# Kernel tuning notes

Measured on AMD Instinct MI355X. Metric: run time of the kernel, lower is better.

The kernel has to match this reference:

```python
import jax, jax.numpy as jnp
import numpy as np

HEADS, DIM_HEAD, LANDMARKS, PINV_ITERS = 8, 64, 256, 6
SCALE = DIM_HEAD ** -0.5
D, L, B, N_IN = 512, 768, 4, 6170


def dwconv(x, w, b, ph, pw):
    # x: [B,C,H,W]; w: [C,1,kh,kw] depthwise (groups=C)
    C = x.shape[1]
    y = jax.lax.conv_general_dilated(x, w, (1, 1), ((ph, ph), (pw, pw)),
                                     feature_group_count=C,
                                     dimension_numbers=('NCHW', 'OIHW', 'NCHW'))
    if b is not None:
        y = y + b[None, :, None, None]
    return y


def layer_norm(x, g, b, eps=1e-5):
    mu = x.mean(-1, keepdims=True)
    var = jnp.mean((x - mu) ** 2, -1, keepdims=True)
    return (x - mu) * jax.lax.rsqrt(var + eps) * g + b


def pinv_iter(a, iters):
    # Moore-Penrose iterative pseudo-inverse (lucidrains), global max normalization
    col = jnp.abs(a).sum(-1).max()
    row = jnp.abs(a).sum(-2).max()
    z = jnp.swapaxes(a, -1, -2) / (col * row)
    I = jnp.eye(a.shape[-1], dtype=a.dtype)
    for _ in range(iters):
        az = a @ z
        z = 0.25 * z @ (13 * I - az @ (15 * I - az @ (7 * I - az)))
    return z


def nystrom_attention(x, qkv_w, out_w, out_b, res_w):
    b, n, _ = x.shape
    m = LANDMARKS
    pad = (m - n % m) % m
    xp = jnp.pad(x, ((0, 0), (pad, 0), (0, 0)))  # pad at front, like F.pad
    N = n + pad
    q, k, v = jnp.split(xp @ qkv_w, 3, axis=-1)
    to_heads = lambda t: t.reshape(b, N, HEADS, DIM_HEAD).transpose(0, 2, 1, 3)
    q, k, v = to_heads(q) * SCALE, to_heads(k), to_heads(v)
    l = N // m
    q_l = q.reshape(b, HEADS, m, l, DIM_HEAD).mean(3)  # landmark means
    k_l = k.reshape(b, HEADS, m, l, DIM_HEAD).mean(3)
    sim1 = jnp.einsum('bhnd,bhmd->bhnm', q, k_l)
    sim2 = jnp.einsum('bhid,bhjd->bhij', q_l, k_l)
    sim3 = jnp.einsum('bhmd,bhnd->bhmn', q_l, k)
    a1 = jax.nn.softmax(sim1, -1)
    a2 = jax.nn.softmax(sim2, -1)
    a3 = jax.nn.softmax(sim3, -1)
    out = (a1 @ pinv_iter(a2, PINV_ITERS)) @ (a3 @ v)
    out = out + dwconv(v, res_w, None, 16, 0)  # depthwise (33,1) conv over seq per head
    out = out.transpose(0, 2, 1, 3).reshape(b, N, HEADS * DIM_HEAD)
    out = out @ out_w + out_b
    return out[:, -n:]


def ppeg(x, w7, b7, w5, b5, w3, b3, H, W):
    Bx, _, C = x.shape
    cls = x[:, :1]
    feat = x[:, 1:].transpose(0, 2, 1).reshape(Bx, C, H, W)
    y = feat + dwconv(feat, w7, b7, 3, 3) + dwconv(feat, w5, b5, 2, 2) + dwconv(feat, w3, b3, 1, 1)
    y = y.reshape(Bx, C, H * W).transpose(0, 2, 1)
    return jnp.concatenate([cls, y], axis=1)


def setup_inputs() -> dict:
    key = jax.random.key(0)
    ks = jax.random.split(key, 24)
    nrm = lambda k, shape, s=0.02: jax.random.normal(k, shape, jnp.float32) * s
    zeros = lambda *s: jnp.zeros(s, jnp.float32)
    ones = lambda *s: jnp.ones(s, jnp.float32)
    return {
        'x': jax.random.normal(ks[0], (B, N_IN, L), jnp.float32),
        'fc1_w': nrm(ks[1], (L, D)), 'fc1_b': zeros(D),
        'cls_token': nrm(ks[2], (1, 1, D)),
        'l1_norm_g': ones(D), 'l1_norm_b': zeros(D),
        'l1_qkv_w': nrm(ks[3], (D, 3 * D)), 'l1_out_w': nrm(ks[4], (D, D)), 'l1_out_b': zeros(D),
        'l1_res_w': nrm(ks[5], (HEADS, 1, 33, 1)),
        'ct_w7': nrm(ks[6], (D, 1, 7, 7)), 'ct_b7': zeros(D),
        'ct_w5': nrm(ks[7], (D, 1, 5, 5)), 'ct_b5': zeros(D),
        'ct_w3': nrm(ks[8], (D, 1, 3, 3)), 'ct_b3': zeros(D),
        'pth_w7': nrm(ks[9], (D, 1, 7, 7)), 'pth_b7': zeros(D),
        'pth_w5': nrm(ks[10], (D, 1, 5, 5)), 'pth_b5': zeros(D),
        'pth_w3': nrm(ks[11], (D, 1, 3, 3)), 'pth_b3': zeros(D),
        'l2_norm_g': ones(D), 'l2_norm_b': zeros(D),
        'l2_qkv_w': nrm(ks[12], (D, 3 * D)), 'l2_out_w': nrm(ks[13], (D, D)), 'l2_out_b': zeros(D),
        'l2_res_w': nrm(ks[14], (HEADS, 1, 33, 1)),
        'norm_g': ones(D), 'norm_b': zeros(D),
    }


def reference(x, fc1_w, fc1_b, cls_token,
              l1_norm_g, l1_norm_b, l1_qkv_w, l1_out_w, l1_out_b, l1_res_w,
              ct_w7, ct_b7, ct_w5, ct_b5, ct_w3, ct_b3,
              pth_w7, pth_b7, pth_w5, pth_b5, pth_w3, pth_b3,
              l2_norm_g, l2_norm_b, l2_qkv_w, l2_out_w, l2_out_b, l2_res_w,
              norm_g, norm_b):
    h = jax.nn.relu(x.astype(jnp.float32) @ fc1_w + fc1_b)  # [B,N,D]
    h_ct = h[:, 10:10 + 160, :]
    h_pth = h[:, 10 + 160:, :]
    # square-pad each modality (static shapes -> Python ints)
    Hc = h_ct.shape[1]
    sc = int(np.ceil(np.sqrt(Hc)))
    h_ct = jnp.concatenate([h_ct, h_ct[:, :sc * sc - Hc, :]], 1)
    n_ct = h_ct.shape[1]
    Hp = h_pth.shape[1]
    sp = int(np.ceil(np.sqrt(Hp)))
    h_pth = jnp.concatenate([h_pth, h_pth[:, :sp * sp - Hp, :]], 1)
    h = jnp.concatenate([h[:, :10, :], h_ct, h_pth], 1)
    Bx = h.shape[0]
    cls = jnp.broadcast_to(cls_token, (Bx, 1, cls_token.shape[-1]))
    h = jnp.concatenate([cls, h], 1)
    # layer 1
    h = h + nystrom_attention(layer_norm(h, l1_norm_g, l1_norm_b), l1_qkv_w, l1_out_w, l1_out_b, l1_res_w)
    # PPEG per modality
    hc = jnp.concatenate([h[:, :1, :], h[:, 1 + 10:1 + 10 + n_ct, :]], 1)
    hp = jnp.concatenate([h[:, :1, :], h[:, 1 + 10 + n_ct:, :]], 1)
    hc = ppeg(hc, ct_w7, ct_b7, ct_w5, ct_b5, ct_w3, ct_b3, sc, sc)
    hp = ppeg(hp, pth_w7, pth_b7, pth_w5, pth_b5, pth_w3, pth_b3, sp, sp)
    h = jnp.concatenate([h[:, :1 + 10, :], hc[:, 1:, :], hp[:, 1:, :]], 1)
    # layer 2
    h = h + nystrom_attention(layer_norm(h, l2_norm_g, l2_norm_b), l2_qkv_w, l2_out_w, l2_out_b, l2_res_w)
    return layer_norm(h, norm_g, norm_b)[:, 0]
```

## Files before the change

### kernel.cpp

```cpp
#include <hip/hip_runtime.h>
#include <hip/hip_bf16.h>
#include <cstdint>

#define B_   4
#define NTOK 6264
#define NPAD 6400
#define D_   512
#define NH   8
#define NLM  256
#define N0   6170
#define PADF (NPAD - NTOK)
#define MFC1 24704
#define QE   ((long long)NPAD * 1536)

typedef __attribute__((ext_vector_type(8))) short short8_t;
typedef __attribute__((ext_vector_type(4))) float float4_t;

__device__ __forceinline__ ushort f2b(float x){
  __hip_bfloat16 h = __float2bfloat16(x); return *(ushort*)&h;
}
__device__ __forceinline__ float b2f(ushort u){
  __hip_bfloat16 h = *(__hip_bfloat16*)&u; return __bfloat162float(h);
}
__device__ __forceinline__ float gload(const void* p, int bf, long long i){
  return bf ? __bfloat162float(((const __hip_bfloat16*)p)[i]) : ((const float*)p)[i];
}
__device__ __forceinline__ void atomicMaxF(float* a, float v){
  atomicMax((int*)a, __float_as_int(v));
}
__device__ __forceinline__ void gl_lds16(const void* g, void* l){
  __builtin_amdgcn_global_load_lds(
      (const __attribute__((address_space(1))) void*)g,
      (__attribute__((address_space(3))) void*)l, 16, 0, 0);
}

struct GB {
  const __hip_bfloat16* A; const __hip_bfloat16* Bm; void* C; const float* bias;
  int M, N, K, lda, ldb, ldc;
  long long aSO, aSI; int aIn;
  long long bSO, bSI; int bIn;
  long long cSO, cSI; int cIn;
  float beta; int cbf, relu, ksp, klen;
};

template<int BN>
__global__ __launch_bounds__(256) void gemm_bt(GB p){
  __shared__ __align__(16) __hip_bfloat16 As[128*64];
  __shared__ __align__(16) __hip_bfloat16 Bs[BN*64];
  int zz = blockIdx.z;
  int z = zz / p.ksp, ks = zz - z*p.ksp;
  int k0 = ks * p.klen;
  int kend = k0 + p.klen; if (kend > p.K) kend = p.K;
  const __hip_bfloat16* A  = p.A  + (long long)(z/p.aIn)*p.aSO + (long long)(z%p.aIn)*p.aSI;
  const __hip_bfloat16* Bm = p.Bm + (long long)(z/p.bIn)*p.bSO + (long long)(z%p.bIn)*p.bSI;
  long long cOff = (long long)(z/p.cIn)*p.cSO + (long long)(z%p.cIn)*p.cSI;
  int rowBase = blockIdx.y*128, colBase = blockIdx.x*BN;
  int t = threadIdx.x, lane = t & 63;
  int wv = __builtin_amdgcn_readfirstlane(t >> 6);
  int lm = lane & 15, lq = lane >> 4;
  int dr = lane >> 3, dc = lane & 7;
  constexpr int NF = (BN == 128) ? 4 : 2;
  int wm = (wv >> 1) * 64;
  int wn = (BN == 128) ? (wv & 1) * 64 : (wv & 1) * 32;
  float4_t acc[4][NF];
  #pragma unroll
  for (int mi = 0; mi < 4; mi++)
    #pragma unroll
    for (int nf = 0; nf < NF; nf++) acc[mi][nf] = (float4_t)0.f;

  for (int kb = k0; kb < kend; kb += 64){
    #pragma unroll
    for (int d = 0; d < 4; d++){
      int rg = wv*4 + d;
      int row = rg*8 + dr;
      int cc = dc ^ (row & 7);
      gl_lds16(A + (long long)(rowBase + row)*p.lda + kb + cc*8, &As[rg*8*64]);
    }
    #pragma unroll
    for (int d = 0; d < BN/32; d++){
      int rg = wv*(BN/32) + d;
      int row = rg*8 + dr;
      int cc = dc ^ (row & 7);
      gl_lds16(Bm + (long long)(colBase + row)*p.ldb + kb + cc*8, &Bs[rg*8*64]);
    }
    __syncthreads();
    short8_t af[2][4]; short8_t bfv[2][NF];
    #pragma unroll
    for (int ks2 = 0; ks2 < 2; ks2++){
      #pragma unroll
      for (int mi = 0; mi < 4; mi++){
        int r = wm + mi*16 + lm;
        int s = (ks2*4 + lq) ^ (r & 7);
        af[ks2][mi] = *(const short8_t*)&As[r*64 + s*8];
      }
      #pragma unroll
      for (int nf = 0; nf < NF; nf++){
        int r = wn + nf*16 + lm;
        int s = (ks2*4 + lq) ^ (r & 7);
        bfv[ks2][nf] = *(const short8_t*)&Bs[r*64 + s*8];
      }
    }
    #pragma unroll
    for (int ks2 = 0; ks2 < 2; ks2++)
      #pragma unroll
      for (int mi = 0; mi < 4; mi++)
        #pragma unroll
        for (int nf = 0; nf < NF; nf++)
          acc[mi][nf] = __builtin_amdgcn_mfma_f32_16x16x32_bf16(af[ks2][mi], bfv[ks2][nf], acc[mi][nf], 0, 0, 0);
    __syncthreads();
  }
  #pragma unroll
  for (int mi = 0; mi < 4; mi++){
    #pragma unroll
    for (int nf = 0; nf < NF; nf++){
      int c = colBase + wn + nf*16 + lm;
      #pragma unroll
      for (int r = 0; r < 4; r++){
        int m = rowBase + wm + mi*16 + lq*4 + r;
        if (m >= p.M) continue;
        float v = p.beta * acc[mi][nf][r];
        long long ci = cOff + (long long)m*p.ldc + c;
        if (p.ksp > 1){
          atomicAdd((float*)p.C + ci, v);
        } else {
          if (p.bias) v += p.bias[c];
          if (p.relu) v = fmaxf(v, 0.f);
          if (p.cbf) ((__hip_bfloat16*)p.C)[ci] = __float2bfloat16(v);
          else       ((float*)p.C)[ci] = v;
        }
      }
    }
  }
}

struct GS {
  const __hip_bfloat16* A; const __hip_bfloat16* B;
  __hip_bfloat16* outN; __hip_bfloat16* outT;
  long long PS;
  float scale, alphaT, sT;
};

__global__ __launch_bounds__(256) void gemm_bts(GS p){
  __shared__ __align__(16) __hip_bfloat16 Ah[64*64];
  __shared__ __align__(16) __hip_bfloat16 Al[64*64];
  __shared__ __align__(16) __hip_bfloat16 Bh[64*64];
  __shared__ __align__(16) __hip_bfloat16 Bl[64*64];
  int z = blockIdx.z;
  long long zo = (long long)z * 65536;
  const __hip_bfloat16* A = p.A + zo;
  const __hip_bfloat16* B = p.B + zo;
  int rowBase = blockIdx.y*64, colBase = blockIdx.x*64;
  int t = threadIdx.x, lane = t & 63;
  int wv = __builtin_amdgcn_readfirstlane(t >> 6);
  int lm = lane & 15, lq = lane >> 4;
  int dr = lane >> 3, dc = lane & 7;
  int wm = (wv >> 1) * 32, wn = (wv & 1) * 32;
  float4_t acc[2][2];
  #pragma unroll
  for (int mi = 0; mi < 2; mi++){ acc[mi][0] = (float4_t)0.f; acc[mi][1] = (float4_t)0.f; }

  for (int kb = 0; kb < 256; kb += 64){
    #pragma unroll
    for (int d = 0; d < 2; d++){
      int rg = wv*2 + d;
      int row = rg*8 + dr;
      int cc = dc ^ (row & 7);
      gl_lds16(A +        (long long)(rowBase + row)*256 + kb + cc*8, &Ah[rg*8*64]);
      gl_lds16(A + p.PS + (long long)(rowBase + row)*256 + kb + cc*8, &Al[rg*8*64]);
      gl_lds16(B +        (long long)(colBase + row)*256 + kb + cc*8, &Bh[rg*8*64]);
      gl_lds16(B + p.PS + (long long)(colBase + row)*256 + kb + cc*8, &Bl[rg*8*64]);
    }
    __syncthreads();
    #pragma unroll
    for (int ks2 = 0; ks2 < 2; ks2++){
      short8_t ah[2], al2[2], bh[2], bl2[2];
      #pragma unroll
      for (int mi = 0; mi < 2; mi++){
        int r = wm + mi*16 + lm;
        int s = (ks2*4 + lq) ^ (r & 7);
        ah[mi]  = *(const short8_t*)&Ah[r*64 + s*8];
        al2[mi] = *(const short8_t*)&Al[r*64 + s*8];
      }
      #pragma unroll
      for (int nf = 0; nf < 2; nf++){
        int r = wn + nf*16 + lm;
        int s = (ks2*4 + lq) ^ (r & 7);
        bh[nf]  = *(const short8_t*)&Bh[r*64 + s*8];
        bl2[nf] = *(const short8_t*)&Bl[r*64 + s*8];
      }
      #pragma unroll
      for (int mi = 0; mi < 2; mi++)
        #pragma unroll
        for (int nf = 0; nf < 2; nf++){
          acc[mi][nf] = __builtin_amdgcn_mfma_f32_16x16x32_bf16(ah[mi],  bh[nf],  acc[mi][nf], 0, 0, 0);
          acc[mi][nf] = __builtin_amdgcn_mfma_f32_16x16x32_bf16(ah[mi],  bl2[nf], acc[mi][nf], 0, 0, 0);
          acc[mi][nf] = __builtin_amdgcn_mfma_f32_16x16x32_bf16(al2[mi], bh[nf],  acc[mi][nf], 0, 0, 0);
        }
    }
    __syncthreads();
  }
  #pragma unroll
  for (int mi = 0; mi < 2; mi++){
    #pragma unroll
    for (int nf = 0; nf < 2; nf++){
      int c = colBase + wn + nf*16 + lm;
      #pragma unroll
      for (int r = 0; r < 4; r++){
        int m = rowBase + wm + mi*16 + lq*4 + r;
        float v = p.scale * acc[mi][nf][r];
        if (p.outN){
          __hip_bfloat16 hi = __float2bfloat16(v);
          p.outN[zo + (long long)m*256 + c] = hi;
          p.outN[p.PS + zo + (long long)m*256 + c] = __float2bfloat16(v - __bfloat162float(hi));
        }
        if (p.outT){
          float w = p.alphaT * (m == c ? 1.f : 0.f) + p.sT * v;
          __hip_bfloat16 hi = __float2bfloat16(w);
          p.outT[zo + (long long)c*256 + m] = hi;
          p.outT[p.PS + zo + (long long)c*256 + m] = __float2bfloat16(w - __bfloat162float(hi));
        }
      }
    }
  }
}

__global__ __launch_bounds__(256) void sim1_fused(const __hip_bfloat16* QKV,
    const __hip_bfloat16* KL, const __hip_bfloat16* ZVT, float* OUT1){
  __shared__ __align__(16) __hip_bfloat16 Ps[64*256];
  int z = blockIdx.y, b = z >> 3, h = z & 7;
  int n0 = blockIdx.x * 64;
  int t = threadIdx.x, lane = t & 63;
  int wv = __builtin_amdgcn_readfirstlane(t >> 6);
  int lm = lane & 15, lq = lane >> 4;
  const __hip_bfloat16* Qb = QKV + (long long)b*QE + h*64;
  const __hip_bfloat16* Kb = KL + (long long)z*NLM*64;
  const __hip_bfloat16* Zb = ZVT + (long long)z*64*256;

  float4_t sacc[16];
  #pragma unroll
  for (int nf = 0; nf < 16; nf++) sacc[nf] = (float4_t)0.f;
  int qrow = n0 + wv*16 + lm;
  #pragma unroll
  for (int ks = 0; ks < 2; ks++){
    short8_t a = *(const short8_t*)(Qb + (long long)qrow*1536 + ks*32 + lq*8);
    #pragma unroll
    for (int nf = 0; nf < 16; nf++){
      short8_t bb = *(const short8_t*)(Kb + (nf*16 + lm)*64 + ks*32 + lq*8);
      sacc[nf] = __builtin_amdgcn_mfma_f32_16x16x32_bf16(a, bb, sacc[nf], 0, 0, 0);
    }
  }
  #pragma unroll
  for (int reg = 0; reg < 4; reg++){
    float mx = -1e30f;
    #pragma unroll
    for (int nf = 0; nf < 16; nf++){
      sacc[nf][reg] *= 0.125f;
      mx = fmaxf(mx, sacc[nf][reg]);
    }
    #pragma unroll
    for (int m = 1; m <= 8; m <<= 1) mx = fmaxf(mx, __shfl_xor(mx, m));
    float sum = 0.f;
    #pragma unroll
    for (int nf = 0; nf < 16; nf++){
      float e = __expf(sacc[nf][reg] - mx);
      sacc[nf][reg] = e; sum += e;
    }
    #pragma unroll
    for (int m = 1; m <= 8; m <<= 1) sum += __shfl_xor(sum, m);
    float inv = 1.f / sum;
    int row = wv*16 + lq*4 + reg;
    #pragma unroll
    for (int nf = 0; nf < 16; nf++){
      int col = nf*16 + lm;
      int chunk = (col >> 3) ^ (row & 7);
      Ps[row*256 + chunk*8 + (col & 7)] = __float2bfloat16(sacc[nf][reg] * inv);
    }
  }
  float4_t oacc[4];
  #pragma unroll
  for (int nf = 0; nf < 4; nf++) oacc[nf] = (float4_t)0.f;
  int prow = wv*16 + lm;
  #pragma unroll
  for (int ks = 0; ks < 8; ks++){
    int chunk = (ks*4 + lq) ^ (lm & 7);
    short8_t a = *(const short8_t*)&Ps[prow*256 + chunk*8];
    #pragma unroll
    for (int nf = 0; nf < 4; nf++){
      short8_t bb = *(const short8_t*)(Zb + (nf*16 + lm)*256 + ks*32 + lq*8);
      oacc[nf] = __builtin_amdgcn_mfma_f32_16x16x32_bf16(a, bb, oacc[nf], 0, 0, 0);
    }
  }
  #pragma unroll
  for (int nf = 0; nf < 4; nf++){
    #pragma unroll
    for (int reg = 0; reg < 4; reg++){
      int tok = n0 + wv*16 + lq*4 + reg;
      OUT1[((long long)b*NPAD + tok)*D_ + h*64 + nf*16 + lm] = oacc[nf][reg];
    }
  }
}

template<int LEN>
__global__ __launch_bounds__(256) void softmax_rows_b(__hip_bfloat16* S){
  constexpr int VPT = LEN / 256;
  __hip_bfloat16* p = S + (long long)blockIdx.x * LEN;
  int t = threadIdx.x;
  float v[VPT]; float m = -1e30f;
  #pragma unroll
  for (int q = 0; q < VPT; q++){ v[q] = __bfloat162float(p[t + 256*q]); m = fmaxf(m, v[q]); }
  __shared__ float red[256];
  red[t] = m; __syncthreads();
  for (int s = 128; s; s >>= 1){ if (t < s) red[t] = fmaxf(red[t], red[t+s]); __syncthreads(); }
  m = red[0]; __syncthreads();
  float sum = 0.f;
  #pragma unroll
  for (int q = 0; q < VPT; q++){ v[q] = __expf(v[q] - m); sum += v[q]; }
  red[t] = sum; __syncthreads();
  for (int s = 128; s; s >>= 1){ if (t < s) red[t] += red[t+s]; __syncthreads(); }
  float inv = 1.f / red[0];
  #pragma unroll
  for (int q = 0; q < VPT; q++) p[t + 256*q] = __float2bfloat16(v[q] * inv);
}

__global__ __launch_bounds__(256) void softmax256_split(float* S, __hip_bfloat16* P, long long PS){
  long long row = blockIdx.x;
  float* p = S + row * 256;
  int t = threadIdx.x;
  float v = p[t];
  __shared__ float red[256];
  red[t] = v; __syncthreads();
  for (int s = 128; s; s >>= 1){ if (t < s) red[t] = fmaxf(red[t], red[t+s]); __syncthreads(); }
  float m = red[0]; __syncthreads();
  float e = __expf(v - m);
  red[t] = e; __syncthreads();
  for (int s = 128; s; s >>= 1){ if (t < s) red[t] += red[t+s]; __syncthreads(); }
  float r = e / red[0];
  p[t] = r;
  __hip_bfloat16 hi = __float2bfloat16(r);
  P[row*256 + t] = hi;
  P[PS + row*256 + t] = __float2bfloat16(r - __bfloat162float(hi));
}

__global__ __launch_bounds__(256) void ln_pad(const float* H, __hip_bfloat16* X,
                                              const float* g, const float* bb){
  int p = blockIdx.x, b = blockIdx.y, t = threadIdx.x;
  __hip_bfloat16* xo = X + ((long long)b * NPAD + p) * D_;
  if (p < PADF){ xo[t] = __float2bfloat16(0.f); xo[t + 256] = __float2bfloat16(0.f); return; }
  const float* hi = H + ((long long)b * NTOK + (p - PADF)) * D_;
  float x0 = hi[t], x1 = hi[t + 256];
  __shared__ float r1[256], r2[256];
  r1[t] = x0 + x1; r2[t] = x0*x0 + x1*x1;
  __syncthreads();
  for (int s = 128; s; s >>= 1){ if (t < s){ r1[t] += r1[t+s]; r2[t] += r2[t+s]; } __syncthreads(); }
  float mu = r1[0] * (1.f / D_);
  float var = r2[0] * (1.f / D_) - mu*mu;
  float rs = rsqrtf(var + 1e-5f);
  xo[t]       = __float2bfloat16((x0 - mu) * rs * g[t]       + bb[t]);
  xo[t + 256] = __float2bfloat16((x1 - mu) * rs * g[t + 256] + bb[t + 256]);
}

__global__ __launch_bounds__(256) void final_ln(const float* H, const float* g,
                                                const float* bb, float* out){
  int b = blockIdx.x, t = threadIdx.x;
  const float* hi = H + (long long)b * NTOK * D_;
  float x0 = hi[t], x1 = hi[t + 256];
  __shared__ float r1[256], r2[256];
  r1[t] = x0 + x1; r2[t] = x0*x0 + x1*x1;
  __syncthreads();
  for (int s = 128; s; s >>= 1){ if (t < s){ r1[t] += r1[t+s]; r2[t] += r2[t+s]; } __syncthreads(); }
  float mu = r1[0] * (1.f / D_);
  float var = r2[0] * (1.f / D_) - mu*mu;
  float rs = rsqrtf(var + 1e-5f);
  out[b*D_ + t]       = (x0 - mu) * rs * g[t]       + bb[t];
  out[b*D_ + t + 256] = (x1 - mu) * rs * g[t + 256] + bb[t + 256];
}

__global__ __launch_bounds__(256) void build_h(const float* h0, const float* cls, float* H){
  int tpos = blockIdx.x, b = blockIdx.y, t = threadIdx.x;
  float* dst = H + ((long long)b * NTOK + tpos) * D_;
  if (tpos == 0){ dst[t] = cls[t]; dst[t + 256] = cls[t + 256]; return; }
  int i = tpos - 1, src;
  if (i < 10)        src = i;
  else if (i < 179){ int j = i - 10;  src = 10  + (j < 160  ? j : j - 160);  }
  else             { int j = i - 179; src = 170 + (j < 6000 ? j : j - 6000); }
  const float* s = h0 + ((long long)b * N0 + src) * D_;
  dst[t] = s[t]; dst[t + 256] = s[t + 256];
}

__global__ __launch_bounds__(256) void cvt_pad_x(const float* x, __hip_bfloat16* Xb){
  int row = blockIdx.x, t = threadIdx.x;
  __hip_bfloat16* o = Xb + (long long)row * 768;
  if (row >= B_*N0){ o[t] = __float2bfloat16(0.f); o[t+256] = __float2bfloat16(0.f); o[t+512] = __float2bfloat16(0.f); return; }
  const float* s = x + (long long)row * 768;
  o[t]     = __float2bfloat16(s[t]);
  o[t+256] = __float2bfloat16(s[t+256]);
  o[t+512] = __float2bfloat16(s[t+512]);
}

__global__ __launch_bounds__(256) void tr_cvt(const void* in, int inbf, int ldin,
    long long iSO, long long iSI, int iIn, __hip_bfloat16* outp, long long oSO,
    int R, int C){
  __shared__ float sm[32][33];
  int z = blockIdx.z;
  long long ib = (long long)(z/iIn)*iSO + (long long)(z%iIn)*iSI;
  int r0 = blockIdx.y*32, c0 = blockIdx.x*32;
  int tx = threadIdx.x & 31, ty = threadIdx.x >> 5;
  for (int rr = ty; rr < 32; rr += 8)
    sm[rr][tx] = gload(in, inbf, ib + (long long)(r0+rr)*ldin + c0 + tx);
  __syncthreads();
  for (int cc = ty; cc < 32; cc += 8)
    outp[z*oSO + (long long)(c0+cc)*R + r0 + tx] = __float2bfloat16(sm[tx][cc]);
}

__global__ __launch_bounds__(256) void landmarks2(const __hip_bfloat16* QKV,
                                                  __hip_bfloat16* QL, __hip_bfloat16* KL){
  int j = blockIdx.x, b = blockIdx.y, t = threadIdx.x;
  const __hip_bfloat16* base = QKV + ((long long)b * NPAD + j*25) * 1536;
  float q0 = 0.f, q1 = 0.f, k0 = 0.f, k1 = 0.f;
  #pragma unroll 5
  for (int i = 0; i < 25; i++){
    const __hip_bfloat16* row = base + (long long)i*1536;
    q0 += __bfloat162float(row[t]);
    q1 += __bfloat162float(row[t + 256]);
    k0 += __bfloat162float(row[512 + t]);
    k1 += __bfloat162float(row[512 + t + 256]);
  }
  int h0 = t >> 6, d0 = t & 63;
  int h1 = (t + 256) >> 6, d1 = (t + 256) & 63;
  QL[((long long)(b*8 + h0) * NLM + j) * 64 + d0] = __float2bfloat16(q0 * 0.005f);
  QL[((long long)(b*8 + h1) * NLM + j) * 64 + d1] = __float2bfloat16(q1 * 0.005f);
  KL[((long long)(b*8 + h0) * NLM + j) * 64 + d0] = __float2bfloat16(k0 * 0.04f);
  KL[((long long)(b*8 + h1) * NLM + j) * 64 + d1] = __float2bfloat16(k1 * 0.04f);
}

__global__ void init_sc(float* sc){ sc[0] = 0.f; sc[1] = 0.f; }
__global__ __launch_bounds__(256) void fillz(float* p, int n){
  int i = blockIdx.x*256 + threadIdx.x; if (i < n) p[i] = 0.f;
}

__global__ __launch_bounds__(256) void colsum_max(const float* A2, float* sc){
  int z = blockIdx.x, t = threadIdx.x;
  const float* a = A2 + (long long)z * 65536;
  float s = 0.f;
  for (int i = 0; i < 256; i++) s += fabsf(a[i*256 + t]);
  __shared__ float red[256];
  red[t] = s; __syncthreads();
  for (int st = 128; st; st >>= 1){ if (t < st) red[t] = fmaxf(red[t], red[t+st]); __syncthreads(); }
  if (t == 0) atomicMaxF(sc + 0, red[0]);
}

__global__ __launch_bounds__(256) void rowsum_max(const float* A2, float* sc){
  int z = blockIdx.x, t = threadIdx.x, w = t >> 6, l = t & 63;
  const float* a = A2 + (long long)z * 65536;
  float mx = 0.f;
  for (int i = w*64; i < (w+1)*64; i++){
    float s = fabsf(a[i*256 + l]) + fabsf(a[i*256 + l + 64])
            + fabsf(a[i*256 + l + 128]) + fabsf(a[i*256 + l + 192]);
    for (int m = 32; m; m >>= 1) s += __shfl_xor(s, m);
    mx = fmaxf(mx, s);
  }
  __shared__ float red[4];
  if (l == 0) red[w] = mx;
  __syncthreads();
  if (t == 0) atomicMaxF(sc + 1, fmaxf(fmaxf(red[0], red[1]), fmaxf(red[2], red[3])));
}

__global__ __launch_bounds__(256) void zinit_split(const float* A2,
    __hip_bfloat16* ZN, __hip_bfloat16* ZT, long long PS, const float* sc){
  int j = blockIdx.x, z = blockIdx.y, i = threadIdx.x;
  float inv = 1.f / (sc[0] * sc[1]);
  float v = A2[(long long)z*65536 + i*256 + j] * inv;
  __hip_bfloat16 hi = __float2bfloat16(v);
  __hip_bfloat16 lo = __float2bfloat16(v - __bfloat162float(hi));
  long long zo = (long long)z*65536;
  ZN[zo + j*256 + i] = hi; ZN[PS + zo + j*256 + i] = lo;
  ZT[zo + i*256 + j] = hi; ZT[PS + zo + i*256 + j] = lo;
}

__global__ __launch_bounds__(256) void dwconv_cvt2(const __hip_bfloat16* QKV, const float* rw,
                                                   const float* OUT1, __hip_bfloat16* OUT1b){
  int t = threadIdx.x;
  int n = blockIdx.x*4 + (t >> 6);
  int b = blockIdx.y;
  int ch0 = (t & 63) * 8;
  int h = (t & 63) >> 3;
  float w[33];
  #pragma unroll
  for (int k = 0; k < 33; k++) w[k] = rw[h*33 + k];
  float acc[8] = {};
  const __hip_bfloat16* Vb = QKV + (long long)b * NPAD * 1536 + 1024 + ch0;
  #pragma unroll
  for (int k = 0; k < 33; k++){
    int nn = n + k - 16;
    if (nn < 0 || nn >= NPAD) continue;
    short8_t v8 = *(const short8_t*)(Vb + (long long)nn * 1536);
    #pragma unroll
    for (int j = 0; j < 8; j++) acc[j] += w[k] * b2f((ushort)v8[j]);
  }
  long long idx = ((long long)b * NPAD + n) * D_ + ch0;
  float4 o0 = *(const float4*)(OUT1 + idx);
  float4 o1 = *(const float4*)(OUT1 + idx + 4);
  short8_t o;
  o[0] = (short)f2b(o0.x + acc[0]); o[1] = (short)f2b(o0.y + acc[1]);
  o[2] = (short)f2b(o0.z + acc[2]); o[3] = (short)f2b(o0.w + acc[3]);
  o[4] = (short)f2b(o1.x + acc[4]); o[5] = (short)f2b(o1.y + acc[5]);
  o[6] = (short)f2b(o1.z + acc[6]); o[7] = (short)f2b(o1.w + acc[7]);
  *(short8_t*)((ushort*)OUT1b + idx) = o;
}

__global__ __launch_bounds__(512) void resid_add(float* H, const float* O2, const float* ob){
  int i = blockIdx.x, b = blockIdx.y, t = threadIdx.x;
  H[((long long)b * NTOK + i) * D_ + t] +=
      O2[((long long)b * NPAD + i + PADF) * D_ + t] + ob[t];
}

__global__ __launch_bounds__(256) void transpose_w(const float* w, float* wt, int KK){
  int i = blockIdx.x*256 + threadIdx.x;
  if (i < 512*KK){ int ch = i / KK, k = i - ch*KK; wt[(long long)k*512 + ch] = w[i]; }
}

__global__ __launch_bounds__(256) void ppeg_tiled(const float* H, float* P,
    const float* t7, const float* t5, const float* t3,
    const float* b7, const float* b5, const float* b3,
    int base, int W, int tilesX){
  __shared__ float smem[196*32];
  int ty0 = (blockIdx.x / tilesX) * 8, tx0 = (blockIdx.x % tilesX) * 8;
  int c0 = blockIdx.y * 32, b = blockIdx.z;
  int t = threadIdx.x, ch = t & 31, y = t >> 5;
  int cc = c0 + ch;
  const float* Hb = H + ((long long)b * NTOK + base) * D_ + cc;
  for (int i = y; i < 196; i += 8){
    int py = i / 14, px = i - py*14;
    int yy = ty0 + py - 3, xx = tx0 + px - 3;
    smem[i*32 + ch] = (yy >= 0 && yy < W && xx >= 0 && xx < W)
                      ? Hb[(long long)(yy*W + xx) * D_] : 0.f;
  }
  __syncthreads();
  float acc[8];
  float bsum = b7[cc] + b5[cc] + b3[cc];
  #pragma unroll
  for (int x = 0; x < 8; x++) acc[x] = bsum;
  #pragma unroll
  for (int r = 0; r < 7; r++){
    float v[14];
    #pragma unroll
    for (int xx = 0; xx < 14; xx++) v[xx] = smem[((y + r)*14 + xx)*32 + ch];
    #pragma unroll
    for (int kx = 0; kx < 7; kx++){
      float w = t7[(r*7 + kx)*512 + cc];
      #pragma unroll
      for (int x = 0; x < 8; x++) acc[x] += w * v[x + kx];
    }
    if (r >= 1 && r <= 5){
      #pragma unroll
      for (int kx = 0; kx < 5; kx++){
        float w = t5[((r-1)*5 + kx)*512 + cc];
        #pragma unroll
        for (int x = 0; x < 8; x++) acc[x] += w * v[x + kx + 1];
      }
    }
    if (r >= 2 && r <= 4){
      #pragma unroll
      for (int kx = 0; kx < 3; kx++){
        float w = t3[((r-2)*3 + kx)*512 + cc];
        #pragma unroll
        for (int x = 0; x < 8; x++) acc[x] += w * v[x + kx + 2];
      }
    }
    if (r == 3){
      #pragma unroll
      for (int x = 0; x < 8; x++) acc[x] += v[x + 3];
    }
  }
  int gy = ty0 + y;
  if (gy < W){
    #pragma unroll
    for (int x = 0; x < 8; x++){
      int gx = tx0 + x;
      if (gx < W)
        P[((long long)b * W * W + gy*W + gx) * D_ + cc] = acc[x];
    }
  }
}

__global__ __launch_bounds__(512) void ppeg_copy(float* H, const float* P, int base, int W){
  int pos = blockIdx.x, b = blockIdx.y, t = threadIdx.x;
  H[((long long)b * NTOK + base + pos) * D_ + t] = P[((long long)b * W * W + pos) * D_ + t];
}

static void gemmB(hipStream_t st, int BN,
                  const __hip_bfloat16* A, int lda, long long aSO, long long aSI, int aIn,
                  const __hip_bfloat16* Bm, int ldb, long long bSO, long long bSI, int bIn,
                  void* C, int ldc, long long cSO, long long cSI, int cIn, int cbf,
                  int M, int N, int K, int batch,
                  const float* bias, float beta, int relu, int ksp = 1, int klen = 0){
  GB p;
  p.A = A; p.Bm = Bm; p.C = C; p.bias = bias;
  p.M = M; p.N = N; p.K = K; p.lda = lda; p.ldb = ldb; p.ldc = ldc;
  p.aSO = aSO; p.aSI = aSI; p.aIn = aIn;
  p.bSO = bSO; p.bSI = bSI; p.bIn = bIn;
  p.cSO = cSO; p.cSI = cSI; p.cIn = cIn; p.cbf = cbf;
  p.beta = beta; p.relu = relu; p.ksp = ksp; p.klen = (klen > 0) ? klen : K;
  dim3 g(N/BN, (M + 127)/128, batch * ksp), b(256);
  if (BN == 128) gemm_bt<128><<<g, b, 0, st>>>(p);
  else           gemm_bt<64><<<g, b, 0, st>>>(p);
}

static void gemmS(hipStream_t st, const ushort* A, const ushort* B,
                  ushort* oN, ushort* oT, float scale, float alphaT, float sT){
  GS p;
  p.A = (const __hip_bfloat16*)A; p.B = (const __hip_bfloat16*)B;
  p.outN = (__hip_bfloat16*)oN; p.outT = (__hip_bfloat16*)oT;
  p.PS = 2097152; p.scale = scale; p.alphaT = alphaT; p.sT = sT;
  dim3 g(4, 4, 32), b(256);
  gemm_bts<<<g, b, 0, st>>>(p);
}

extern "C" void kernel_launch(void* const* d_in, const int* in_sizes, int n_in,
                              void* d_out, int out_size, void* d_ws, size_t ws_size,
                              hipStream_t stream){
  const float* x      = (const float*)d_in[0];
  const float* fc1_w  = (const float*)d_in[1];
  const float* fc1_b  = (const float*)d_in[2];
  const float* cls    = (const float*)d_in[3];
  const float* l1_ng  = (const float*)d_in[4];
  const float* l1_nb  = (const float*)d_in[5];
  const float* l1_qkv = (const float*)d_in[6];
  const float* l1_ow  = (const float*)d_in[7];
  const float* l1_ob  = (const float*)d_in[8];
  const float* l1_rw  = (const float*)d_in[9];
  const float* ct_w7  = (const float*)d_in[10];
  const float* ct_b7  = (const float*)d_in[11];
  const float* ct_w5  = (const float*)d_in[12];
  const float* ct_b5  = (const float*)d_in[13];
  const float* ct_w3  = (const float*)d_in[14];
  const float* ct_b3  = (const float*)d_in[15];
  const float* pt_w7  = (const float*)d_in[16];
  const float* pt_b7  = (const float*)d_in[17];
  const float* pt_w5  = (const float*)d_in[18];
  const float* pt_b5  = (const float*)d_in[19];
  const float* pt_w3  = (const float*)d_in[20];
  const float* pt_b3  = (const float*)d_in[21];
  const float* l2_ng  = (const float*)d_in[22];
  const float* l2_nb  = (const float*)d_in[23];
  const float* l2_qkv = (const float*)d_in[24];
  const float* l2_ow  = (const float*)d_in[25];
  const float* l2_ob  = (const float*)d_in[26];
  const float* l2_rw  = (const float*)d_in[27];
  const float* nrm_g  = (const float*)d_in[28];
  const float* nrm_b  = (const float*)d_in[29];
  float* out = (float*)d_out;

  float* ws    = (float*)d_ws;
  float* H     = ws;
  float* BUF   = H + 12828672;
  float* QKVr  = BUF + 13107200;
  float* QLf   = QKVr + 19660800;
  float* KLf   = QLf + 262144;
  float* AV    = KLf + 262144;
  float* AVTf  = AV + 524288;
  float* ZVf   = AVTf + 262144;
  float* ZVTf  = ZVf + 262144;
  float* WQf   = ZVTf + 262144;
  float* WFf   = WQf + 393216;
  float* WOf   = WFf + 196608;
  float* PWT   = WOf + 131072;
  float* SC    = PWT + 84992;
  float* SIMC  = SC + 8;
  float* tc7 = PWT, *tc5 = tc7 + 49*512, *tc3 = tc5 + 25*512;
  float* tp7 = tc3 + 9*512, *tp5 = tp7 + 49*512, *tp3 = tp5 + 25*512;

  long long fixedB = (long long)((char*)SIMC - (char*)ws);
  long long availB = (long long)ws_size - fixedB;
  int G = (availB >= 104857600LL) ? 32 : (availB >= 52428800LL) ? 16 : 8;

  float*  A2   = BUF;
  ushort* a2P  = (ushort*)(BUF + 2097152);
  ushort* zn_N = (ushort*)(BUF + 4194304);
  ushort* zn_T = (ushort*)(BUF + 6291456);
  ushort* zc_N = (ushort*)(BUF + 8388608);
  ushort* zc_T = (ushort*)(BUF + 10485760);
  ushort* azP  = (ushort*)SIMC;
  ushort* w1T  = (ushort*)SIMC + 4194304;
  ushort* w2T  = (ushort*)SIMC + 8388608;

  __hip_bfloat16* Xb    = (__hip_bfloat16*)QKVr;
  __hip_bfloat16* QKV   = (__hip_bfloat16*)QKVr;
  float*          PROJ  = QKVr;
  __hip_bfloat16* XLNb  = (__hip_bfloat16*)BUF;
  __hip_bfloat16* VT    = (__hip_bfloat16*)BUF;
  __hip_bfloat16* SIMCb = (__hip_bfloat16*)SIMC;
  __hip_bfloat16* OUT1b = (__hip_bfloat16*)SIMC;
  __hip_bfloat16* QLb   = (__hip_bfloat16*)QLf;
  __hip_bfloat16* KLb   = (__hip_bfloat16*)KLf;
  __hip_bfloat16* AVT   = (__hip_bfloat16*)AVTf;
  __hip_bfloat16* Zvb   = (__hip_bfloat16*)ZVf;
  __hip_bfloat16* ZVT   = (__hip_bfloat16*)ZVTf;
  __hip_bfloat16* WqkvT = (__hip_bfloat16*)WQf;
  __hip_bfloat16* Wfc1T = (__hip_bfloat16*)WFf;
  __hip_bfloat16* WoutT = (__hip_bfloat16*)WOf;

  transpose_w<<<(512*49+255)/256, 256, 0, stream>>>(ct_w7, tc7, 49);
  transpose_w<<<(512*25+255)/256, 256, 0, stream>>>(ct_w5, tc5, 25);
  transpose_w<<<(512* 9+255)/256, 256, 0, stream>>>(ct_w3, tc3,  9);
  transpose_w<<<(512*49+255)/256, 256, 0, stream>>>(pt_w7, tp7, 49);
  transpose_w<<<(512*25+255)/256, 256, 0, stream>>>(pt_w5, tp5, 25);
  transpose_w<<<(512* 9+255)/256, 256, 0, stream>>>(pt_w3, tp3,  9);
  tr_cvt<<<dim3(512/32, 768/32, 1), 256, 0, stream>>>(fc1_w, 0, 512, 0,0,1, Wfc1T, 0, 768, 512);

  cvt_pad_x<<<MFC1, 256, 0, stream>>>(x, Xb);
  gemmB(stream, 128, Xb, 768, 0,0,1, Wfc1T, 768, 0,0,1, BUF, 512, 0,0,1,0,
        MFC1, 512, 768, 1, fc1_b, 1.f, 1);
  build_h<<<dim3(NTOK, B_), 256, 0, stream>>>(BUF, cls, H);

  auto attn_layer = [&](const float* ng, const float* nb, const float* qkvw,
                        const float* outw, const float* outb, const float* resw){
    tr_cvt<<<dim3(1536/32, 512/32, 1), 256, 0, stream>>>(qkvw, 0, 1536, 0,0,1, WqkvT, 0, 512, 1536);
    tr_cvt<<<dim3(512/32, 512/32, 1), 256, 0, stream>>>(outw, 0, 512, 0,0,1, WoutT, 0, 512, 512);
    ln_pad<<<dim3(NPAD, B_), 256, 0, stream>>>(H, XLNb, ng, nb);
    gemmB(stream, 128, XLNb, 512, 0,0,1, WqkvT, 512, 0,0,1, QKV, 1536, 0,0,1,1,
          B_*NPAD, 1536, 512, 1, nullptr, 1.f, 0);
    landmarks2<<<dim3(NLM, B_), 256, 0, stream>>>(QKV, QLb, KLb);
    gemmB(stream, 128, QLb, 64, 16384,0,1, KLb, 64, 16384,0,1, A2, 256, 65536,0,1,0,
          256, 256, 64, 32, nullptr, 1.f, 0);
    softmax256_split<<<B_*NH*NLM, 256, 0, stream>>>(A2, (__hip_bfloat16*)a2P, 2097152);
    init_sc<<<1, 1, 0, stream>>>(SC);
    colsum_max<<<B_*NH, 256, 0, stream>>>(A2, SC);
    rowsum_max<<<B_*NH, 256, 0, stream>>>(A2, SC);
    zinit_split<<<dim3(256, 32), 256, 0, stream>>>(A2, (__hip_bfloat16*)zc_N,
          (__hip_bfloat16*)zc_T, 2097152, SC);
    ushort *cN = zc_N, *cT = zc_T, *nN = zn_N, *nT = zn_T;
    for (int it = 0; it < 6; it++){
      gemmS(stream, a2P, cT, azP, w1T, 1.f, 7.f, -1.f);
      gemmS(stream, azP, w1T, nullptr, w2T, 1.f, 15.f, -1.f);
      gemmS(stream, azP, w2T, nullptr, w1T, 1.f, 13.f, -1.f);
      gemmS(stream, cN, w1T, nN, nT, 0.25f, 0.f, 1.f);
      ushort* s;
      s = cN; cN = nN; nN = s;
      s = cT; cT = nT; nT = s;
    }
    const __hip_bfloat16* Zcb = (const __hip_bfloat16*)cN;
    tr_cvt<<<dim3(64/32, NPAD/32, 32), 256, 0, stream>>>(QKV + 1024, 1, 1536,
          QE, 64, 8, VT, (long long)64*NPAD, NPAD, 64);
    fillz<<<2048, 256, 0, stream>>>(AV, 524288);
    for (int c0 = 0; c0 < 32; c0 += G){
      int b0 = c0 >> 3;
      const __hip_bfloat16* Kp = QKV + (long long)b0*QE + 512;
      gemmB(stream, 128, QLb + (long long)c0*16384, 64, 16384,0,1,
            Kp, 1536, QE,64,8,
            SIMCb, NPAD, (long long)256*NPAD,0,1,1,
            256, NPAD, 64, G, nullptr, 1.f, 0);
      softmax_rows_b<NPAD><<<G*NLM, 256, 0, stream>>>(SIMCb);
      gemmB(stream, 64, SIMCb, NPAD, (long long)256*NPAD,0,1,
            VT + (long long)c0*64*NPAD, NPAD, (long long)64*NPAD,0,1,
            AV + (long long)c0*16384, 64, 16384,0,1,0,
            256, 64, NPAD, G, nullptr, 1.f, 0, 10, 640);
    }
    tr_cvt<<<dim3(64/32, 256/32, 32), 256, 0, stream>>>(AV, 0, 64, 16384,0,1,
          AVT, 16384, 256, 64);
    gemmB(stream, 64, Zcb, 256, 65536,0,1, AVT, 256, 16384,0,1,
          Zvb, 64, 16384,0,1,1, 256, 64, 256, 32, nullptr, 1.f, 0);
    tr_cvt<<<dim3(64/32, 256/32, 32), 256, 0, stream>>>(Zvb, 1, 64, 16384,0,1,
          ZVT, 16384, 256, 64);
    sim1_fused<<<dim3(NPAD/64, 32), 256, 0, stream>>>(QKV, KLb, ZVT, BUF);
    dwconv_cvt2<<<dim3(NPAD/4, B_), 256, 0, stream>>>(QKV, resw, BUF, OUT1b);
    gemmB(stream, 128, OUT1b, 512, 0,0,1, WoutT, 512, 0,0,1, PROJ, 512, 0,0,1,0,
          B_*NPAD, 512, 512, 1, nullptr, 1.f, 0);
    resid_add<<<dim3(NTOK, B_), 512, 0, stream>>>(H, PROJ, outb);
  };

  attn_layer(l1_ng, l1_nb, l1_qkv, l1_ow, l1_ob, l1_rw);

  ppeg_tiled<<<dim3(4, 16, B_), 256, 0, stream>>>(H, BUF, tc7, tc5, tc3, ct_b7, ct_b5, ct_b3, 11, 13, 2);
  ppeg_copy<<<dim3(169, B_), 512, 0, stream>>>(H, BUF, 11, 13);
  ppeg_tiled<<<dim3(100, 16, B_), 256, 0, stream>>>(H, BUF, tp7, tp5, tp3, pt_b7, pt_b5, pt_b3, 180, 78, 10);
  ppeg_copy<<<dim3(6084, B_), 512, 0, stream>>>(H, BUF, 180, 78);

  attn_layer(l2_ng, l2_nb, l2_qkv, l2_ow, l2_ob, l2_rw);

  final_ln<<<B_, 256, 0, stream>>>(H, nrm_g, nrm_b, out);
}
```

Before: 2.537 ms.

## Fuse sim3 softmax-attention with split-K online softmax and stage PPEG weights in LDS

Replaces the landmark-query attention path (a3 @ v), which materialized a 256×6400 score matrix per head, ran a row softmax and then a separate GEMM, with a single flash-style kernel. That kernel computes scores, keeps an online softmax and accumulates P·V across four key splits, and a small merge kernel then combines the partials. This removes the large score-matrix round trip to global memory and several launches. Separately, the PPEG depthwise conv kernel now preloads its filter weights and biases into shared memory and loads the input tile as float4. The fused grid is small (512 blocks, each looping over 25 key tiles), so occupancy is limited.

```diff
diff --git a/kernel.cpp b/kernel.cpp
--- a/kernel.cpp
+++ b/kernel.cpp
@@ -224,6 +224,131 @@
   }
 }
 
+__global__ __launch_bounds__(256) void sim3_fused(const __hip_bfloat16* QKV,
+    const __hip_bfloat16* QL, const __hip_bfloat16* VT, float* AVp, float* MLp){
+  __shared__ __align__(16) __hip_bfloat16 Ks[64*64];
+  __shared__ __align__(16) __hip_bfloat16 Ps[4*16*64];
+  int z = blockIdx.y, b = z >> 3, h = z & 7;
+  int r0 = blockIdx.x * 64;
+  int ksp = blockIdx.z;
+  int t = threadIdx.x, lane = t & 63;
+  int wv = __builtin_amdgcn_readfirstlane(t >> 6);
+  int lm = lane & 15, lq = lane >> 4;
+  int dr = lane >> 3, dc = lane & 7;
+  const __hip_bfloat16* Kb = QKV + (long long)b*QE + h*64 + 512;
+  const __hip_bfloat16* Vb = VT + (long long)z*64*NPAD;
+
+  short8_t aq[2];
+  #pragma unroll
+  for (int ks = 0; ks < 2; ks++)
+    aq[ks] = *(const short8_t*)(QL + (long long)z*NLM*64 + (r0 + wv*16 + lm)*64 + ks*32 + lq*8);
+
+  float m_run[4], l_run[4];
+  float4_t oacc[4];
+  #pragma unroll
+  for (int r = 0; r < 4; r++){ m_run[r] = -1e30f; l_run[r] = 0.f; }
+  #pragma unroll
+  for (int nf = 0; nf < 4; nf++) oacc[nf] = (float4_t)0.f;
+
+  int kbase = ksp * (NPAD/4);
+  for (int kt = 0; kt < (NPAD/4)/64; kt++){
+    int k0 = kbase + kt*64;
+    __syncthreads();
+    #pragma unroll
+    for (int d = 0; d < 2; d++){
+      int rg = wv*2 + d;
+      int row = rg*8 + dr;
+      int cc = dc ^ (row & 7);
+      gl_lds16(Kb + (long long)(k0 + row)*1536 + cc*8, &Ks[rg*8*64]);
+    }
+    __syncthreads();
+    float4_t sacc[4];
+    #pragma unroll
+    for (int nf = 0; nf < 4; nf++) sacc[nf] = (float4_t)0.f;
+    #pragma unroll
+    for (int ks = 0; ks < 2; ks++){
+      #pragma unroll
+      for (int nf = 0; nf < 4; nf++){
+        int r = nf*16 + lm;
+        int s = (ks*4 + lq) ^ (r & 7);
+        short8_t bb = *(const short8_t*)&Ks[r*64 + s*8];
+        sacc[nf] = __builtin_amdgcn_mfma_f32_16x16x32_bf16(aq[ks], bb, sacc[nf], 0, 0, 0);
+      }
+    }
+    #pragma unroll
+    for (int reg = 0; reg < 4; reg++){
+      float mt = fmaxf(fmaxf(sacc[0][reg], sacc[1][reg]), fmaxf(sacc[2][reg], sacc[3][reg]));
+      #pragma unroll
+      for (int mm = 1; mm <= 8; mm <<= 1) mt = fmaxf(mt, __shfl_xor(mt, mm));
+      float mnew = fmaxf(m_run[reg], mt);
+      float alpha = __expf(m_run[reg] - mnew);
+      float sum = 0.f;
+      #pragma unroll
+      for (int nf = 0; nf < 4; nf++){
+        float e = __expf(sacc[nf][reg] - mnew);
+        sacc[nf][reg] = e; sum += e;
+      }
+      #pragma unroll
+      for (int mm = 1; mm <= 8; mm <<= 1) sum += __shfl_xor(sum, mm);
+      l_run[reg] = l_run[reg]*alpha + sum;
+      m_run[reg] = mnew;
+      #pragma unroll
+      for (int nf = 0; nf < 4; nf++) oacc[nf][reg] *= alpha;
+      int row = lq*4 + reg;
+      #pragma unroll
+      for (int nf = 0; nf < 4; nf++){
+        int col = nf*16 + lm;
+        Ps[(wv*16 + row)*64 + (((col>>3) ^ (row&7))*8) + (col&7)] = __float2bfloat16(sacc[nf][reg]);
+      }
+    }
+    #pragma unroll
+    for (int ks = 0; ks < 2; ks++){
+      int s = (ks*4 + lq) ^ (lm & 7);
+      short8_t ap = *(const short8_t*)&Ps[(wv*16 + lm)*64 + s*8];
+      #pragma unroll
+      for (int nf = 0; nf < 4; nf++){
+        short8_t bb = *(const short8_t*)(Vb + (long long)(nf*16 + lm)*NPAD + k0 + ks*32 + lq*8);
+        oacc[nf] = __builtin_amdgcn_mfma_f32_16x16x32_bf16(ap, bb, oacc[nf], 0, 0, 0);
+      }
+    }
+  }
+  long long zb = (long long)(ksp*32 + z);
+  #pragma unroll
+  for (int nf = 0; nf < 4; nf++){
+    #pragma unroll
+    for (int reg = 0; reg < 4; reg++){
+      int row = r0 + wv*16 + lq*4 + reg;
+      AVp[zb*16384 + row*64 + nf*16 + lm] = oacc[nf][reg];
+    }
+  }
+  if (lm == 0){
+    #pragma unroll
+    for (int reg = 0; reg < 4; reg++){
+      int row = r0 + wv*16 + lq*4 + reg;
+      MLp[(zb*256 + row)*2 + 0] = m_run[reg];
+      MLp[(zb*256 + row)*2 + 1] = l_run[reg];
+    }
+  }
+}
+
+__global__ __launch_bounds__(256) void av_merge(const float* AVp, const float* MLp, float* AV){
+  int i = blockIdx.x*256 + threadIdx.x;
+  int d = i & 63, row = (i >> 6) & 255, z = i >> 14;
+  float M = -1e30f;
+  #pragma unroll
+  for (int s = 0; s < 4; s++) M = fmaxf(M, MLp[((long long)(s*32+z)*256 + row)*2]);
+  float osum = 0.f, lsum = 0.f;
+  #pragma unroll
+  for (int s = 0; s < 4; s++){
+    float m = MLp[((long long)(s*32+z)*256 + row)*2];
+    float l = MLp[((long long)(s*32+z)*256 + row)*2 + 1];
+    float w = __expf(m - M);
+    osum += w * AVp[(long long)(s*32+z)*16384 + row*64 + d];
+    lsum += w * l;
+  }
+  AV[(long long)z*16384 + row*64 + d] = osum / lsum;
+}
+
 __global__ __launch_bounds__(256) void sim1_fused(const __hip_bfloat16* QKV,
     const __hip_bfloat16* KL, const __hip_bfloat16* ZVT, float* OUT1){
   __shared__ __align__(16) __hip_bfloat16 Ps[64*256];
@@ -298,28 +423,6 @@
       OUT1[((long long)b*NPAD + tok)*D_ + h*64 + nf*16 + lm] = oacc[nf][reg];
     }
   }
-}
-
-template<int LEN>
-__global__ __launch_bounds__(256) void softmax_rows_b(__hip_bfloat16* S){
-  constexpr int VPT = LEN / 256;
-  __hip_bfloat16* p = S + (long long)blockIdx.x * LEN;
-  int t = threadIdx.x;
-  float v[VPT]; float m = -1e30f;
-  #pragma unroll
-  for (int q = 0; q < VPT; q++){ v[q] = __bfloat162float(p[t + 256*q]); m = fmaxf(m, v[q]); }
-  __shared__ float red[256];
-  red[t] = m; __syncthreads();
-  for (int s = 128; s; s >>= 1){ if (t < s) red[t] = fmaxf(red[t], red[t+s]); __syncthreads(); }
-  m = red[0]; __syncthreads();
-  float sum = 0.f;
-  #pragma unroll
-  for (int q = 0; q < VPT; q++){ v[q] = __expf(v[q] - m); sum += v[q]; }
-  red[t] = sum; __syncthreads();
-  for (int s = 128; s; s >>= 1){ if (t < s) red[t] += red[t+s]; __syncthreads(); }
-  float inv = 1.f / red[0];
-  #pragma unroll
-  for (int q = 0; q < VPT; q++) p[t + 256*q] = __float2bfloat16(v[q] * inv);
 }
 
 __global__ __launch_bounds__(256) void softmax256_split(float* S, __hip_bfloat16* P, long long PS){
@@ -434,9 +537,6 @@
 }
 
 __global__ void init_sc(float* sc){ sc[0] = 0.f; sc[1] = 0.f; }
-__global__ __launch_bounds__(256) void fillz(float* p, int n){
-  int i = blockIdx.x*256 + threadIdx.x; if (i < n) p[i] = 0.f;
-}
 
 __global__ __launch_bounds__(256) void colsum_max(const float* A2, float* sc){
   int z = blockIdx.x, t = threadIdx.x;
@@ -524,20 +624,35 @@
     const float* b7, const float* b5, const float* b3,
     int base, int W, int tilesX){
   __shared__ float smem[196*32];
+  __shared__ float wsm[83*32 + 32];
   int ty0 = (blockIdx.x / tilesX) * 8, tx0 = (blockIdx.x % tilesX) * 8;
   int c0 = blockIdx.y * 32, b = blockIdx.z;
   int t = threadIdx.x, ch = t & 31, y = t >> 5;
   int cc = c0 + ch;
-  const float* Hb = H + ((long long)b * NTOK + base) * D_ + cc;
-  for (int i = y; i < 196; i += 8){
-    int py = i / 14, px = i - py*14;
-    int yy = ty0 + py - 3, xx = tx0 + px - 3;
-    smem[i*32 + ch] = (yy >= 0 && yy < W && xx >= 0 && xx < W)
-                      ? Hb[(long long)(yy*W + xx) * D_] : 0.f;
+  for (int i = t; i < 83*32; i += 256){
+    int k = i >> 5, c = c0 + (i & 31);
+    float w;
+    if (k < 49)      w = t7[k*512 + c];
+    else if (k < 74) w = t5[(k-49)*512 + c];
+    else             w = t3[(k-74)*512 + c];
+    wsm[i] = w;
+  }
+  if (t < 32) wsm[83*32 + t] = b7[c0+t] + b5[c0+t] + b3[c0+t];
+  {
+    const float* Hb = H + ((long long)b * NTOK + base) * D_ + c0;
+    for (int q = t; q < 1568; q += 256){
+      int pos = q >> 3, c4 = (q & 7) * 4;
+      int py = pos / 14, px = pos - py*14;
+      int yy = ty0 + py - 3, xx = tx0 + px - 3;
+      float4 v = make_float4(0.f, 0.f, 0.f, 0.f);
+      if (yy >= 0 && yy < W && xx >= 0 && xx < W)
+        v = *(const float4*)(Hb + (long long)(yy*W + xx)*D_ + c4);
+      *(float4*)&smem[pos*32 + c4] = v;
+    }
   }
   __syncthreads();
   float acc[8];
-  float bsum = b7[cc] + b5[cc] + b3[cc];
+  float bsum = wsm[83*32 + ch];
   #pragma unroll
   for (int x = 0; x < 8; x++) acc[x] = bsum;
   #pragma unroll
@@ -547,14 +662,14 @@
     for (int xx = 0; xx < 14; xx++) v[xx] = smem[((y + r)*14 + xx)*32 + ch];
     #pragma unroll
     for (int kx = 0; kx < 7; kx++){
-      float w = t7[(r*7 + kx)*512 + cc];
+      float w = wsm[(r*7 + kx)*32 + ch];
       #pragma unroll
       for (int x = 0; x < 8; x++) acc[x] += w * v[x + kx];
     }
     if (r >= 1 && r <= 5){
       #pragma unroll
       for (int kx = 0; kx < 5; kx++){
-        float w = t5[((r-1)*5 + kx)*512 + cc];
+        float w = wsm[(49 + (r-1)*5 + kx)*32 + ch];
         #pragma unroll
         for (int x = 0; x < 8; x++) acc[x] += w * v[x + kx + 1];
       }
@@ -562,7 +677,7 @@
     if (r >= 2 && r <= 4){
       #pragma unroll
       for (int kx = 0; kx < 3; kx++){
-        float w = t3[((r-2)*3 + kx)*512 + cc];
+        float w = wsm[(74 + (r-2)*3 + kx)*32 + ch];
         #pragma unroll
         for (int x = 0; x < 8; x++) acc[x] += w * v[x + kx + 2];
       }
@@ -670,10 +785,6 @@
   float* tc7 = PWT, *tc5 = tc7 + 49*512, *tc3 = tc5 + 25*512;
   float* tp7 = tc3 + 9*512, *tp5 = tp7 + 49*512, *tp3 = tp5 + 25*512;
 
-  long long fixedB = (long long)((char*)SIMC - (char*)ws);
-  long long availB = (long long)ws_size - fixedB;
-  int G = (availB >= 104857600LL) ? 32 : (availB >= 52428800LL) ? 16 : 8;
-
   float*  A2   = BUF;
   ushort* a2P  = (ushort*)(BUF + 2097152);
   ushort* zn_N = (ushort*)(BUF + 4194304);
@@ -683,13 +794,14 @@
   ushort* azP  = (ushort*)SIMC;
   ushort* w1T  = (ushort*)SIMC + 4194304;
   ushort* w2T  = (ushort*)SIMC + 8388608;
+  float*  AVp  = SIMC;
+  float*  MLp  = SIMC + 2097152;
 
   __hip_bfloat16* Xb    = (__hip_bfloat16*)QKVr;
   __hip_bfloat16* QKV   = (__hip_bfloat16*)QKVr;
   float*          PROJ  = QKVr;
   __hip_bfloat16* XLNb  = (__hip_bfloat16*)BUF;
   __hip_bfloat16* VT    = (__hip_bfloat16*)BUF;
-  __hip_bfloat16* SIMCb = (__hip_bfloat16*)SIMC;
   __hip_bfloat16* OUT1b = (__hip_bfloat16*)SIMC;
   __hip_bfloat16* QLb   = (__hip_bfloat16*)QLf;
   __hip_bfloat16* KLb   = (__hip_bfloat16*)KLf;
@@ -742,20 +854,8 @@
     const __hip_bfloat16* Zcb = (const __hip_bfloat16*)cN;
     tr_cvt<<<dim3(64/32, NPAD/32, 32), 256, 0, stream>>>(QKV + 1024, 1, 1536,
           QE, 64, 8, VT, (long long)64*NPAD, NPAD, 64);
-    fillz<<<2048, 256, 0, stream>>>(AV, 524288);
-    for (int c0 = 0; c0 < 32; c0 += G){
-      int b0 = c0 >> 3;
-      const __hip_bfloat16* Kp = QKV + (long long)b0*QE + 512;
-      gemmB(stream, 128, QLb + (long long)c0*16384, 64, 16384,0,1,
-            Kp, 1536, QE,64,8,
-            SIMCb, NPAD, (long long)256*NPAD,0,1,1,
-            256, NPAD, 64, G, nullptr, 1.f, 0);
-      softmax_rows_b<NPAD><<<G*NLM, 256, 0, stream>>>(SIMCb);
-      gemmB(stream, 64, SIMCb, NPAD, (long long)256*NPAD,0,1,
-            VT + (long long)c0*64*NPAD, NPAD, (long long)64*NPAD,0,1,
-            AV + (long long)c0*16384, 64, 16384,0,1,0,
-            256, 64, NPAD, G, nullptr, 1.f, 0, 10, 640);
-    }
+    sim3_fused<<<dim3(4, 32, 4), 256, 0, stream>>>(QKV, QLb, VT, AVp, MLp);
+    av_merge<<<2048, 256, 0, stream>>>(AVp, MLp, AV);
     tr_cvt<<<dim3(64/32, 256/32, 32), 256, 0, stream>>>(AV, 0, 64, 16384,0,1,
           AVT, 16384, 256, 64);
     gemmB(stream, 64, Zcb, 256, 65536,0,1, AVT, 256, 16384,0,1,
```

Result: faster. 2.395 ms (-5.6%).
